# Kernel optimization log

Measured on AMD Instinct MI355X. Metric: run time of the kernel, lower is better.

The kernel has to match this reference:

```python
import jax, jax.numpy as jnp
import numpy as np

P = 8          # patch_size
DIM = 256      # embed dim
HEADS = 8
HEAD_DIM = DIM // HEADS
CH = 3
PATCH_DIM = CH * P * P  # 192
INNER = int(4.0 * DIM)  # 1024
SCALE = HEAD_DIM ** -0.5


def sine_pos_embedding(n, c, dtype=jnp.float32):
    # standard 1D sinusoidal position encoding, shape (n, c)
    pos = jnp.arange(n, dtype=jnp.float32)[:, None]            # (n,1)
    div = jnp.exp(jnp.arange(0, c, 2, dtype=jnp.float32) * (-np.log(10000.0) / c))
    pe = jnp.zeros((n, c), dtype=jnp.float32)
    pe = pe.at[:, 0::2].set(jnp.sin(pos * div))
    pe = pe.at[:, 1::2].set(jnp.cos(pos * div))
    return pe.astype(dtype)


def patchify(x):
    # (B,C,H,W) -> (B, n, p1*p2*C), matching 'b c (h p1) (w p2) -> b (h w) (p1 p2 c)'
    B, C, H, W = x.shape
    hp, wp = H // P, W // P
    x = x.reshape(B, C, hp, P, wp, P)
    x = x.transpose(0, 2, 4, 3, 5, 1)        # (B, hp, wp, p1, p2, C)
    return x.reshape(B, hp * wp, P * P * C)


def unpatchify(x, hp, wp):
    # (B, n, p1*p2*C) -> (B, C, H, W)
    B = x.shape[0]
    x = x.reshape(B, hp, wp, P, P, CH)
    x = x.transpose(0, 5, 1, 3, 2, 4)        # (B, C, hp, p1, wp, p2)
    return x.reshape(B, CH, hp * P, wp * P)


def setup_inputs() -> dict:
    key = jax.random.key(0)
    ks = jax.random.split(key, 16)
    B, H, W = 8, 256, 256
    s = 0.02
    img0 = jax.random.normal(ks[0], (B, CH, H, W), dtype=jnp.float32)
    img1 = jax.random.normal(ks[1], (B, CH, H, W), dtype=jnp.float32)
    mask = jax.random.randint(ks[2], (B, 1, H, W), 0, 2).astype(jnp.float32)
    return {
        "img0": img0,
        "img1": img1,
        "mask": mask,
        "w_patch": jax.random.normal(ks[3], (PATCH_DIM, DIM), jnp.float32) * s,
        "b_patch": jnp.zeros((DIM,), jnp.float32),
        "w_kv": jax.random.normal(ks[4], (DIM, 2 * DIM), jnp.float32) * s,
        "b_kv": jnp.zeros((2 * DIM,), jnp.float32),
        "w_qv": jax.random.normal(ks[5], (DIM, 2 * DIM), jnp.float32) * s,
        "b_qv": jnp.zeros((2 * DIM,), jnp.float32),
        "w_fc1": jax.random.normal(ks[6], (DIM, INNER), jnp.float32) * s,
        "b_fc1": jnp.zeros((INNER,), jnp.float32),
        "w_fc2": jax.random.normal(ks[7], (INNER, PATCH_DIM), jnp.float32) * s,
        "b_fc2": jnp.zeros((PATCH_DIM,), jnp.float32),
    }


def reference(img0, img1, mask, w_patch, b_patch, w_kv, b_kv, w_qv, b_qv,
              w_fc1, b_fc1, w_fc2, b_fc2):
    B, C, H, W = img0.shape
    hp, wp = H // P, W // P
    n = hp * wp

    x0 = patchify(img0) @ w_patch + b_patch   # (B, n, dim)
    x1 = patchify(img1) @ w_patch + b_patch
    pe = sine_pos_embedding(n, DIM)
    x0 = x0 + pe
    x1 = x1 + pe

    # img0 -> k, v
    kv = (x0 @ w_kv + b_kv).reshape(B, n, 2, HEADS, HEAD_DIM)
    kv = kv.transpose(2, 0, 3, 1, 4)          # (2, B, heads, n, hd)
    k, v = kv[0], kv[1]

    # img1 -> q (v1 unused in forward, matching torch code)
    qv = (x1 @ w_qv + b_qv).reshape(B, n, 2, DIM).transpose(2, 0, 1, 3)
    q = qv[0].reshape(B, n, HEADS, HEAD_DIM).transpose(0, 2, 1, 3)  # (B, heads, n, hd)

    dots = jnp.einsum('bhqd,bhkd->bhqk', q, k) * SCALE  # (B, heads, n, n)

    # mask: (B,1,H,W) -> per-patch sum -> binary -> additive bias over key dim
    msum = mask.reshape(B, 1, hp, P, wp, P).sum(axis=(3, 5)).reshape(B, 1, n)
    bias = jnp.where(msum > 0, 0.0, -100.0)[:, :, None, :]  # (B,1,1,n)

    attn = jax.nn.softmax(dots + bias, axis=-1)
    out = jnp.einsum('bhqk,bhkd->bhqd', attn, v)
    out = out.transpose(0, 2, 1, 3).reshape(B, n, DIM)

    # mlp2: Linear -> GELU(exact) -> Linear
    h = jax.nn.gelu(out @ w_fc1 + b_fc1, approximate=False)
    res = h @ w_fc2 + b_fc2                   # (B, n, patch_dim)

    return unpatchify(res, hp, wp)            # (B, C, H, W)
```

## Files before the change

kernel.cpp:

```cpp
#include <hip/hip_runtime.h>
#include <cstdint>
#include <cstddef>

typedef __bf16 bf16_t;
typedef uint32_t u32;
typedef __bf16 bf16x4 __attribute__((ext_vector_type(4)));
typedef __bf16 bf16x8 __attribute__((ext_vector_type(8)));
typedef float f32x4 __attribute__((ext_vector_type(4)));
typedef float f32x16 __attribute__((ext_vector_type(16)));

__device__ __forceinline__ void gload_lds16(const bf16_t* g, bf16_t* l) {
  __builtin_amdgcn_global_load_lds((const __attribute__((address_space(1))) void*)g,
                                   (__attribute__((address_space(3))) void*)l,
                                   16, 0, 0);
}

__device__ __forceinline__ f32x4 mfma16(bf16x8 a, bf16x8 b, f32x4 c) {
  return __builtin_amdgcn_mfma_f32_16x16x32_bf16(a, b, c, 0, 0, 0);
}
__device__ __forceinline__ f32x16 mfma32(bf16x8 a, bf16x8 b, f32x16 c) {
  return __builtin_amdgcn_mfma_f32_32x32x16_bf16(a, b, c, 0, 0, 0);
}

#define LOG2E 1.4426950408889634f

__global__ __launch_bounds__(256)
void prep_all(const float* __restrict__ img0, const float* __restrict__ img1,
              const float* __restrict__ mask,
              const float* __restrict__ wp, const float* __restrict__ wkv,
              const float* __restrict__ wqv, const float* __restrict__ wfc1,
              const float* __restrict__ wfc2,
              bf16_t* __restrict__ xp0, bf16_t* __restrict__ xp1,
              float* __restrict__ pe, float* __restrict__ bias,
              bf16_t* __restrict__ wpT, bf16_t* __restrict__ wkvT,
              bf16_t* __restrict__ wqT, bf16_t* __restrict__ wfc1T,
              bf16_t* __restrict__ wfc2T) {
  __shared__ float tl[64 * 65];
  int bid = blockIdx.x, tid = threadIdx.x;
  if (bid < 1536) {
    int imgsel = bid >= 768;
    int t = (bid - (imgsel ? 768 : 0)) * 256 + tid;
    const float* img = imgsel ? img1 : img0;
    bf16_t* xp = imgsel ? xp1 : xp0;
    int wpp = t & 31, p1 = (t >> 5) & 7, hp = (t >> 8) & 31, rest = t >> 13;
    int b = rest / 3, c = rest - b * 3;
    const float* src = img + (((size_t)(b * 3 + c) * 256 + hp * 8 + p1) * 256 + wpp * 8);
    float4 v0 = *(const float4*)src;
    float4 v1 = *(const float4*)(src + 4);
    int row = b * 1024 + hp * 32 + wpp;
    bf16_t* dst = xp + (size_t)row * 192 + p1 * 24 + c;
    dst[0]  = (bf16_t)v0.x; dst[3]  = (bf16_t)v0.y; dst[6]  = (bf16_t)v0.z; dst[9]  = (bf16_t)v0.w;
    dst[12] = (bf16_t)v1.x; dst[15] = (bf16_t)v1.y; dst[18] = (bf16_t)v1.z; dst[21] = (bf16_t)v1.w;
  } else if (bid < 2560) {
    int t = bid - 1536, c = tid;
    int i2 = c & ~1;
    float div = __expf((float)i2 * (-9.210340371976184f / 256.0f));
    float arg = (float)t * div;
    float sv, cv;
    __sincosf(arg, &sv, &cv);
    pe[t * 256 + c] = (c & 1) ? cv : sv;
  } else if (bid < 2592) {
    int g = (bid - 2560) * 256 + tid;
    int b = g >> 10, t = g & 1023, hp = t >> 5, wpp = t & 31;
    const float* mp = mask + ((size_t)b * 256 + hp * 8) * 256 + wpp * 8;
    float s = 0.f;
    #pragma unroll
    for (int p1 = 0; p1 < 8; p1++) {
      float4 a = *(const float4*)(mp + p1 * 256);
      float4 c = *(const float4*)(mp + p1 * 256 + 4);
      s += a.x + a.y + a.z + a.w + c.x + c.y + c.z + c.w;
    }
    bias[g] = (s > 0.f) ? 0.f : (-100.f * LOG2E);
  } else {
    int i = bid - 2592;
    const float* src; bf16_t* dst; int srcN, dstK, NT;
    if (i >= 172) {
      int j = i - 172;
      bf16_t* p = wfc2T + 192 * 1024 + j * 8192 + tid * 32;
      bf16x8 z;
      #pragma unroll
      for (int e = 0; e < 8; e++) z[e] = (bf16_t)0.0f;
      *(bf16x8*)(p) = z; *(bf16x8*)(p + 8) = z;
      *(bf16x8*)(p + 16) = z; *(bf16x8*)(p + 24) = z;
      return;
    }
    if (i < 12)       { src = wp;   dst = wpT;   srcN = 256;  dstK = 192;  NT = 4; }
    else if (i < 44)  { i -= 12;  src = wkv;  dst = wkvT;  srcN = 512;  dstK = 256;  NT = 8; }
    else if (i < 60)  { i -= 44;  src = wqv;  dst = wqT;   srcN = 512;  dstK = 256;  NT = 4; }
    else if (i < 124) { i -= 60;  src = wfc1; dst = wfc1T; srcN = 1024; dstK = 256;  NT = 16; }
    else              { i -= 124; src = wfc2; dst = wfc2T; srcN = 192;  dstK = 1024; NT = 3; }
    int kt = i / NT, nt = i - kt * NT;
    #pragma unroll
    for (int j = 0; j < 4; j++) {
      int r = (tid >> 4) + 16 * j, c = (tid & 15) * 4;
      float4 v = *(const float4*)(src + (size_t)(kt * 64 + r) * srcN + nt * 64 + c);
      tl[r * 65 + c] = v.x; tl[r * 65 + c + 1] = v.y;
      tl[r * 65 + c + 2] = v.z; tl[r * 65 + c + 3] = v.w;
    }
    __syncthreads();
    #pragma unroll
    for (int j = 0; j < 16; j++) {
      int flat = tid + 256 * j;
      int n_l = flat >> 6, k_l = flat & 63;
      dst[(size_t)(nt * 64 + n_l) * dstK + kt * 64 + k_l] = (bf16_t)tl[k_l * 65 + n_l];
    }
  }
}

template<int EPI, int BN>
__global__ __launch_bounds__(256, 3)
void gemm128d(const bf16_t* __restrict__ A_, const bf16_t* __restrict__ A2,
              const bf16_t* __restrict__ Bt_, const bf16_t* __restrict__ Bt2,
              int M, int N, int K,
              const float* __restrict__ bias_, const float* __restrict__ bias2,
              const float* __restrict__ pe,
              bf16_t* __restrict__ out_b, bf16_t* __restrict__ out_b2,
              bf16_t* __restrict__ out_b3, float* __restrict__ out_f) {
  constexpr int NF = BN / 32;
  __shared__ bf16_t alds[4 * 128 * 8];
  __shared__ bf16_t blds[4 * BN * 8];
  const int tid = threadIdx.x;
  const int lane = tid & 63, wid = tid >> 6;
  const int ln15 = lane & 15, hi = lane >> 4;
  const int brow = blockIdx.x * 128;
  int bcol = blockIdx.y * BN;
  const bf16_t* A = A_;
  const bf16_t* Bt = Bt_;
  const float* bias = bias_;
  bool qpart = false;
  if (EPI == 0 && blockIdx.z) A = A2;
  if (EPI == 5 && blockIdx.y >= 4) {
    qpart = true; A = A2; Bt = Bt2; bias = bias2; bcol -= 512;
  }
  const int wr = wid >> 1, wc = wid & 1;

  f32x4 acc[4][NF];
  #pragma unroll
  for (int m = 0; m < 4; m++)
    #pragma unroll
    for (int n = 0; n < NF; n++) acc[m][n] = (f32x4){0.f, 0.f, 0.f, 0.f};

  for (int k0 = 0; k0 < K; k0 += 32) {
    #pragma unroll
    for (int s = 0; s < 2; s++) {
      int c = tid + s * 256; int kb = c >> 7, row = c & 127;
      gload_lds16(A + (size_t)(brow + row) * K + k0 + kb * 8,
                  &alds[(size_t)(s * 256 + wid * 64) * 8]);
    }
    #pragma unroll
    for (int s = 0; s < BN / 64; s++) {
      int c = tid + s * 256; int kb = c / BN, row = c % BN;
      gload_lds16(Bt + (size_t)(bcol + row) * K + k0 + kb * 8,
                  &blds[(size_t)(s * 256 + wid * 64) * 8]);
    }
    __syncthreads();
    bf16x8 bfr[NF];
    #pragma unroll
    for (int n = 0; n < NF; n++)
      bfr[n] = *(const bf16x8*)&blds[(size_t)(hi * BN + wc * (BN / 2) + n * 16 + ln15) * 8];
    #pragma unroll
    for (int m = 0; m < 4; m++) {
      bf16x8 af = *(const bf16x8*)&alds[(size_t)(hi * 128 + wr * 64 + m * 16 + ln15) * 8];
      #pragma unroll
      for (int n = 0; n < NF; n++)
        acc[m][n] = mfma16(af, bfr[n], acc[m][n]);
    }
    __syncthreads();
  }

  #pragma unroll
  for (int m = 0; m < 4; m++) {
    #pragma unroll
    for (int n = 0; n < NF; n++) {
      #pragma unroll
      for (int r = 0; r < 4; r++) {
        int grow = brow + wr * 64 + m * 16 + hi * 4 + r;
        int gcol = bcol + wc * (BN / 2) + n * 16 + ln15;
        float v = acc[m][n][r];
        if (EPI == 0) {
          v += bias[gcol] + pe[(grow & 1023) * 256 + gcol];
          bf16_t* outx = blockIdx.z ? out_b2 : out_b;
          outx[(size_t)grow * N + gcol] = (bf16_t)v;
        } else if (EPI == 5) {
          v += bias[gcol];
          int b = grow >> 10, t = grow & 1023;
          if (!qpart) {
            if (gcol < 256) {
              int h = gcol >> 5, d = gcol & 31;
              out_b[(((size_t)(b * 8 + h) * 1024 + t) << 5) + d] = (bf16_t)v;
            } else {
              int c2 = gcol - 256; int h = c2 >> 5, d = c2 & 31;
              out_b2[(((size_t)(b * 8 + h) * 32 + d) << 10) + t] = (bf16_t)v;
            }
          } else {
            v *= (0.17677669529663687f * LOG2E);
            int h = gcol >> 5, d = gcol & 31;
            out_b3[(((size_t)(b * 8 + h) * 1024 + t) << 5) + d] = (bf16_t)v;
          }
        } else if (EPI == 3) {
          v += bias[gcol];
          float gg = 0.5f * v * (1.0f + erff(v * 0.7071067811865476f));
          out_b[(size_t)grow * N + gcol] = (bf16_t)gg;
        }
      }
    }
  }
}

template<int BN>
__global__ __launch_bounds__(256)
void gemm_fc2(const bf16_t* __restrict__ A, const bf16_t* __restrict__ Bt,
              int M, int N, int K, const float* __restrict__ bias,
              float* __restrict__ out_f) {
  constexpr int NF = BN / 32;
  __shared__ bf16_t alds[2][8 * 64 * 8];
  __shared__ bf16_t blds[2][8 * BN * 8];
  const int tid = threadIdx.x;
  const int lane = tid & 63, wid = tid >> 6;
  const int ln15 = lane & 15, hi = lane >> 4;
  const int brow = blockIdx.x * 64;
  const int bcol = blockIdx.y * BN;
  const int wr = wid >> 1, wc = wid & 1;

  auto stage = [&](int buf, int k0) {
    #pragma unroll
    for (int s = 0; s < 2; s++) {
      int c = tid + s * 256; int kb = c >> 6, row = c & 63;
      gload_lds16(A + (size_t)(brow + row) * K + k0 + kb * 8,
                  &alds[buf][(size_t)(s * 256 + wid * 64) * 8]);
    }
    #pragma unroll
    for (int s = 0; s < BN / 32; s++) {
      int c = tid + s * 256; int kb = c / BN, row = c & (BN - 1);
      gload_lds16(Bt + (size_t)(bcol + row) * K + k0 + kb * 8,
                  &blds[buf][(size_t)(s * 256 + wid * 64) * 8]);
    }
  };

  f32x4 acc[2][NF];
  #pragma unroll
  for (int m = 0; m < 2; m++)
    #pragma unroll
    for (int n = 0; n < NF; n++) acc[m][n] = (f32x4){0.f, 0.f, 0.f, 0.f};

  stage(0, 0);
  __syncthreads();
  int cur = 0;
  const int NT = K >> 6;
  for (int t = 0; t < NT; t++) {
    if (t + 1 < NT) stage(cur ^ 1, (t + 1) << 6);
    bf16x8 af[2][2], bfr[2][NF];
    #pragma unroll
    for (int kk = 0; kk < 2; kk++) {
      #pragma unroll
      for (int m = 0; m < 2; m++)
        af[kk][m] = *(const bf16x8*)&alds[cur][(size_t)((kk * 4 + hi) * 64 + wr * 32 + m * 16 + ln15) * 8];
      #pragma unroll
      for (int n = 0; n < NF; n++)
        bfr[kk][n] = *(const bf16x8*)&blds[cur][(size_t)((kk * 4 + hi) * BN + wc * (BN / 2) + n * 16 + ln15) * 8];
    }
    #pragma unroll
    for (int kk = 0; kk < 2; kk++)
      #pragma unroll
      for (int m = 0; m < 2; m++)
        #pragma unroll
        for (int n = 0; n < NF; n++)
          acc[m][n] = mfma16(af[kk][m], bfr[kk][n], acc[m][n]);
    __syncthreads();
    cur ^= 1;
  }

  #pragma unroll
  for (int m = 0; m < 2; m++) {
    #pragma unroll
    for (int n = 0; n < NF; n++) {
      #pragma unroll
      for (int r = 0; r < 4; r++) {
        int grow = brow + wr * 32 + m * 16 + hi * 4 + r;
        int gcol = bcol + wc * (BN / 2) + n * 16 + ln15;
        float v = acc[m][n][r] + bias[gcol];
        int b = grow >> 10, t = grow & 1023;
        int hp = t >> 5, wpp = t & 31;
        int p = gcol / 3; int c = gcol - p * 3;
        int p1 = p >> 3, p2 = p & 7;
        out_f[(((size_t)(b * 3 + c) * 256 + hp * 8 + p1) * 256) + wpp * 8 + p2] = v;
      }
    }
  }
}

union PW { u32 w[4]; bf16x8 v; };

__device__ __forceinline__ u32 pkbf(float a, float b) {
  union { bf16_t h[2]; u32 w; } u;
  u.h[0] = (bf16_t)a; u.h[1] = (bf16_t)b;
  return u.w;
}

__device__ __forceinline__ void pl32swap(u32& a, u32& b) {
  asm volatile("v_permlane32_swap_b32 %0, %1" : "+v"(a), "+v"(b));
}

#define SMEM_BYTES 32768

__device__ __forceinline__ void stage_kv(const bf16_t* kbase, const bf16_t* vbase,
                                         int ch, char* smem, int cur,
                                         int tid, int wid) {
  bf16_t* kl = (bf16_t*)(smem + cur * 8192);
  bf16_t* vl = (bf16_t*)(smem + 16384 + cur * 8192);
  #pragma unroll
  for (int s = 0; s < 2; s++) {
    int c = tid + s * 256;
    int row = c >> 2, cs = (c & 3) ^ (row & 3);
    gload_lds16(kbase + (size_t)(ch * 128 + row) * 32 + cs * 8,
                kl + (size_t)(s * 256 + wid * 64) * 8);
  }
  #pragma unroll
  for (int s = 0; s < 2; s++) {
    int c = tid + s * 256;
    int row = c >> 4, cs = (c & 15) ^ (row & 15);
    gload_lds16(vbase + (size_t)row * 1024 + ch * 128 + cs * 8,
                vl + (size_t)(s * 256 + wid * 64) * 8);
  }
}

__global__ __launch_bounds__(256, 4)
void attn_kernel(const bf16_t* __restrict__ q, const bf16_t* __restrict__ k,
                 const bf16_t* __restrict__ vt, const float* __restrict__ bias,
                 bf16_t* __restrict__ out) {
  __shared__ __align__(16) char smem[SMEM_BYTES];

  int tid = threadIdx.x, lane = tid & 63, wid = tid >> 6;
  int l31 = lane & 31, g = lane >> 5;
  int x = blockIdx.x & 7, idx = blockIdx.x >> 3;
  int qt = idx & 31;
  int bh = ((idx >> 5) << 3) | x;
  int b = bh >> 3, h = bh & 7;
  int q0 = qt * 32;
  const bf16_t* qp = q + ((size_t)bh * 1024 + q0 + l31) * 32;
  bf16x8 qf0 = *(const bf16x8*)(qp + g * 8);
  bf16x8 qf1 = *(const bf16x8*)(qp + 16 + g * 8);
  const bf16_t* kbase = k + (size_t)bh * 32768;
  const bf16_t* vbase = vt + (size_t)bh * 32768;
  const float* bb = bias + b * 1024;

  f32x16 acc;
  #pragma unroll
  for (int r = 0; r < 16; r++) acc[r] = 0.f;
  float lsum = 0.f;

  stage_kv(kbase, vbase, 0, smem, 0, tid, wid);
  __syncthreads();

  int cur = 0;
  for (int ch = 0; ch < 8; ch++) {
    if (ch < 7) stage_kv(kbase, vbase, ch + 1, smem, cur ^ 1, tid, wid);
    const bf16_t* kl = (const bf16_t*)(smem + cur * 8192);
    const bf16_t* vl = (const bf16_t*)(smem + 16384 + cur * 8192);
    int base = ch * 128 + wid * 32;
    int row0 = wid * 32 + l31;
    bf16x8 kA = *(const bf16x8*)(kl + (size_t)(row0 * 4 + (g ^ (row0 & 3))) * 8);
    bf16x8 kB = *(const bf16x8*)(kl + (size_t)(row0 * 4 + ((2 + g) ^ (row0 & 3))) * 8);
    bf16x8 vA = *(const bf16x8*)(vl + (size_t)(l31 * 16 + ((wid * 4 + g) ^ (l31 & 15))) * 8);
    bf16x8 vB = *(const bf16x8*)(vl + (size_t)(l31 * 16 + ((wid * 4 + 2 + g) ^ (l31 & 15))) * 8);
    f32x4 c0 = *(const f32x4*)(bb + base + 4 * g);
    f32x4 c1 = *(const f32x4*)(bb + base + 8 + 4 * g);
    f32x4 c2 = *(const f32x4*)(bb + base + 16 + 4 * g);
    f32x4 c3 = *(const f32x4*)(bb + base + 24 + 4 * g);
    f32x16 S;
    S[0] = c0[0]; S[1] = c0[1]; S[2] = c0[2]; S[3] = c0[3];
    S[4] = c1[0]; S[5] = c1[1]; S[6] = c1[2]; S[7] = c1[3];
    S[8] = c2[0]; S[9] = c2[1]; S[10] = c2[2]; S[11] = c2[3];
    S[12] = c3[0]; S[13] = c3[1]; S[14] = c3[2]; S[15] = c3[3];
    S = mfma32(kA, qf0, S);
    S = mfma32(kB, qf1, S);
    float p[16];
    #pragma unroll
    for (int r = 0; r < 16; r++) p[r] = exp2f(S[r]);
    lsum += (((p[0] + p[1]) + (p[2] + p[3])) + ((p[4] + p[5]) + (p[6] + p[7]))) +
            (((p[8] + p[9]) + (p[10] + p[11])) + ((p[12] + p[13]) + (p[14] + p[15])));
    u32 w[8];
    #pragma unroll
    for (int j = 0; j < 8; j++) w[j] = pkbf(p[2 * j], p[2 * j + 1]);
    u32 xa = w[2], ya = w[0]; pl32swap(xa, ya);
    u32 xb = w[3], yb = w[1]; pl32swap(xb, yb);
    u32 xc = w[6], yc = w[4]; pl32swap(xc, yc);
    u32 xd = w[7], yd = w[5]; pl32swap(xd, yd);
    PW A0, A1;
    A0.w[0] = g ? xa : w[0];  A0.w[2] = g ? w[2] : ya;
    A0.w[1] = g ? xb : w[1];  A0.w[3] = g ? w[3] : yb;
    A1.w[0] = g ? xc : w[4];  A1.w[2] = g ? w[6] : yc;
    A1.w[1] = g ? xd : w[5];  A1.w[3] = g ? w[7] : yd;
    acc = mfma32(A0.v, vA, acc);
    acc = mfma32(A1.v, vB, acc);
    __syncthreads();
    cur ^= 1;
  }

  float* OL = (float*)smem;
  float* LS = (float*)(smem + 16896);
  #pragma unroll
  for (int r = 0; r < 16; r++) {
    int row = (r & 3) + 8 * (r >> 2) + 4 * g;
    OL[wid * 1056 + row * 33 + l31] = acc[r];
  }
  lsum += __shfl_xor(lsum, 32);
  LS[wid * 32 + l31] = lsum;
  __syncthreads();

  int qq = tid >> 3, d0 = (tid & 7) * 4;
  float l = LS[qq] + LS[32 + qq] + LS[64 + qq] + LS[96 + qq];
  float o0 = 0.f, o1 = 0.f, o2 = 0.f, o3 = 0.f;
  #pragma unroll
  for (int w2 = 0; w2 < 4; w2++) {
    const float* p = &OL[w2 * 1056 + qq * 33 + d0];
    o0 += p[0]; o1 += p[1]; o2 += p[2]; o3 += p[3];
  }
  float linv = 1.f / l;
  bf16x4 ov;
  ov[0] = (bf16_t)(o0 * linv); ov[1] = (bf16_t)(o1 * linv);
  ov[2] = (bf16_t)(o2 * linv); ov[3] = (bf16_t)(o3 * linv);
  *(bf16x4*)(out + ((size_t)b * 1024 + q0 + qq) * 256 + h * 32 + d0) = ov;
}

extern "C" void kernel_launch(void* const* d_in, const int* in_sizes, int n_in,
                              void* d_out, int out_size, void* d_ws, size_t ws_size,
                              hipStream_t stream) {
  (void)in_sizes; (void)n_in; (void)out_size; (void)ws_size;
  const float* img0    = (const float*)d_in[0];
  const float* img1    = (const float*)d_in[1];
  const float* mask    = (const float*)d_in[2];
  const float* w_patch = (const float*)d_in[3];
  const float* b_patch = (const float*)d_in[4];
  const float* w_kv    = (const float*)d_in[5];
  const float* b_kv    = (const float*)d_in[6];
  const float* w_qv    = (const float*)d_in[7];
  const float* b_qv    = (const float*)d_in[8];
  const float* w_fc1   = (const float*)d_in[9];
  const float* b_fc1   = (const float*)d_in[10];
  const float* w_fc2   = (const float*)d_in[11];
  const float* b_fc2   = (const float*)d_in[12];
  float* out = (float*)d_out;

  char* ws = (char*)d_ws;
  float*  pe    = (float*)(ws + 0);
  float*  bias  = (float*)(ws + 1048576);
  bf16_t* wpT   = (bf16_t*)(ws + 1081344);
  bf16_t* wkvT  = (bf16_t*)(ws + 1179648);
  bf16_t* wqT   = (bf16_t*)(ws + 1441792);
  bf16_t* wfc1T = (bf16_t*)(ws + 1572864);
  bf16_t* wfc2T = (bf16_t*)(ws + 2097152);
  bf16_t* xp0   = (bf16_t*)(ws + 2621440);
  bf16_t* xp1   = (bf16_t*)(ws + 5767168);
  bf16_t* x0    = (bf16_t*)(ws + 8912896);
  bf16_t* x1    = (bf16_t*)(ws + 13107200);
  bf16_t* kbuf  = (bf16_t*)(ws + 17301504);
  bf16_t* vtbuf = (bf16_t*)(ws + 21495808);
  bf16_t* qbuf  = (bf16_t*)(ws + 25690112);
  bf16_t* aout  = (bf16_t*)(ws + 29884416);
  bf16_t* hbuf  = (bf16_t*)(ws + 34078720);

  prep_all<<<2772, 256, 0, stream>>>(img0, img1, mask, w_patch, w_kv, w_qv, w_fc1, w_fc2,
                                     xp0, xp1, pe, bias, wpT, wkvT, wqT, wfc1T, wfc2T);

  gemm128d<0, 64><<<dim3(64, 4, 2), 256, 0, stream>>>(xp0, xp1, wpT, nullptr, 8192, 256, 192,
                                                      b_patch, nullptr, pe, x0, x1, nullptr, nullptr);
  gemm128d<5, 128><<<dim3(64, 6), 256, 0, stream>>>(x0, x1, wkvT, wqT, 8192, 512, 256,
                                                    b_kv, b_qv, nullptr, kbuf, vtbuf, qbuf, nullptr);

  attn_kernel<<<2048, 256, 0, stream>>>(qbuf, kbuf, vtbuf, bias, aout);

  gemm128d<3, 128><<<dim3(64, 8), 256, 0, stream>>>(aout, nullptr, wfc1T, nullptr, 8192, 1024, 256,
                                                    b_fc1, nullptr, nullptr, hbuf, nullptr, nullptr, nullptr);
  gemm_fc2<64><<<dim3(128, 3), 256, 0, stream>>>(hbuf, wfc2T, 8192, 256, 1024, b_fc2, out);
}
```

Baseline: 117.1 us.

## Fold patch embedding into KV/Q projections by precomputing combined weights

Because the patch embedding and the KV/Q projections are both linear, the code now multiplies the weights together in a small prep kernel (W_patch·W_kv and W_patch·W_q). It also precomputes the position-embedding-plus-bias term through the projection, giving per-token bias tables. The separate patch-embed GEMM and its x0/x1 intermediate buffers go away, and the projection GEMM now works directly on patch pixels with K=192. This removes one GEMM launch and its memory traffic. In exchange it adds a small prep GEMM, reads larger bias tables in the epilogue, and rounds the combined weights to bf16, which changes numerics slightly.

```diff
diff --git a/kernel.cpp b/kernel.cpp
--- a/kernel.cpp
+++ b/kernel.cpp
@@ -26,13 +26,13 @@
 
 __global__ __launch_bounds__(256)
 void prep_all(const float* __restrict__ img0, const float* __restrict__ img1,
-              const float* __restrict__ mask,
+              const float* __restrict__ mask, const float* __restrict__ b_patch,
               const float* __restrict__ wp, const float* __restrict__ wkv,
               const float* __restrict__ wqv, const float* __restrict__ wfc1,
               const float* __restrict__ wfc2,
               bf16_t* __restrict__ xp0, bf16_t* __restrict__ xp1,
-              float* __restrict__ pe, float* __restrict__ bias,
-              bf16_t* __restrict__ wpT, bf16_t* __restrict__ wkvT,
+              bf16_t* __restrict__ pe1b, float* __restrict__ bias,
+              bf16_t* __restrict__ wpB, bf16_t* __restrict__ wkvT,
               bf16_t* __restrict__ wqT, bf16_t* __restrict__ wfc1T,
               bf16_t* __restrict__ wfc2T) {
   __shared__ float tl[64 * 65];
@@ -58,7 +58,8 @@
     float arg = (float)t * div;
     float sv, cv;
     __sincosf(arg, &sv, &cv);
-    pe[t * 256 + c] = (c & 1) ? cv : sv;
+    float v = ((c & 1) ? cv : sv) + b_patch[c];
+    pe1b[t * 256 + c] = (bf16_t)v;
   } else if (bid < 2592) {
     int g = (bid - 2560) * 256 + tid;
     int b = g >> 10, t = g & 1023, hp = t >> 5, wpp = t & 31;
@@ -67,8 +68,8 @@
     #pragma unroll
     for (int p1 = 0; p1 < 8; p1++) {
       float4 a = *(const float4*)(mp + p1 * 256);
-      float4 c = *(const float4*)(mp + p1 * 256 + 4);
-      s += a.x + a.y + a.z + a.w + c.x + c.y + c.z + c.w;
+      float4 c2 = *(const float4*)(mp + p1 * 256 + 4);
+      s += a.x + a.y + a.z + a.w + c2.x + c2.y + c2.z + c2.w;
     }
     bias[g] = (s > 0.f) ? 0.f : (-100.f * LOG2E);
   } else {
@@ -84,7 +85,18 @@
       *(bf16x8*)(p + 16) = z; *(bf16x8*)(p + 24) = z;
       return;
     }
-    if (i < 12)       { src = wp;   dst = wpT;   srcN = 256;  dstK = 192;  NT = 4; }
+    if (i < 12) {
+      int base = i * 4096 + tid * 16;
+      const float* s4 = wp + base;
+      bf16_t* d = wpB + base;
+      #pragma unroll
+      for (int j = 0; j < 4; j++) {
+        float4 v = *(const float4*)(s4 + j * 4);
+        d[j * 4 + 0] = (bf16_t)v.x; d[j * 4 + 1] = (bf16_t)v.y;
+        d[j * 4 + 2] = (bf16_t)v.z; d[j * 4 + 3] = (bf16_t)v.w;
+      }
+      return;
+    }
     else if (i < 44)  { i -= 12;  src = wkv;  dst = wkvT;  srcN = 512;  dstK = 256;  NT = 8; }
     else if (i < 60)  { i -= 44;  src = wqv;  dst = wqT;   srcN = 512;  dstK = 256;  NT = 4; }
     else if (i < 124) { i -= 60;  src = wfc1; dst = wfc1T; srcN = 1024; dstK = 256;  NT = 16; }
@@ -103,6 +115,75 @@
       int flat = tid + 256 * j;
       int n_l = flat >> 6, k_l = flat & 63;
       dst[(size_t)(nt * 64 + n_l) * dstK + kt * 64 + k_l] = (bf16_t)tl[k_l * 65 + n_l];
+    }
+  }
+}
+
+__global__ __launch_bounds__(256)
+void prep2(const bf16_t* __restrict__ wkvT, const bf16_t* __restrict__ wqT,
+           const bf16_t* __restrict__ wpB, const bf16_t* __restrict__ pe1b,
+           const float* __restrict__ b_kv, const float* __restrict__ b_qv,
+           bf16_t* __restrict__ wpkvT, bf16_t* __restrict__ wpqT,
+           float* __restrict__ pekv, float* __restrict__ peq) {
+  __shared__ bf16_t alds[4 * 64 * 8];
+  __shared__ bf16_t blds[4 * 64 * 8];
+  const int tid = threadIdx.x;
+  const int lane = tid & 63, wid = tid >> 6;
+  const int ln15 = lane & 15, hi = lane >> 4;
+  const int wr = wid >> 1, wc = wid & 1;
+  const int arow = tid & 63, akb = tid >> 6;
+  const int K = 256;
+
+  int t = blockIdx.x;
+  const bf16_t *A, *B;
+  int bx, by, task;
+  if (t < 24)       { task = 0; bx = t / 3;          by = t - 3 * (t / 3);  A = wkvT; B = wpB; }
+  else if (t < 36)  { task = 1; int i = t - 24;  bx = i / 3; by = i - 3 * (i / 3); A = wqT;  B = wpB; }
+  else if (t < 164) { task = 2; int i = t - 36;  bx = i >> 3; by = i & 7;  A = pe1b; B = wkvT; }
+  else              { task = 3; int i = t - 164; bx = i >> 2; by = i & 3;  A = pe1b; B = wqT; }
+  const int brow = bx * 64, bcol = by * 64;
+
+  f32x4 acc[2][2];
+  #pragma unroll
+  for (int m = 0; m < 2; m++)
+    #pragma unroll
+    for (int n = 0; n < 2; n++) acc[m][n] = (f32x4){0.f, 0.f, 0.f, 0.f};
+
+  for (int k0 = 0; k0 < K; k0 += 32) {
+    gload_lds16(A + (size_t)(brow + arow) * K + k0 + akb * 8,
+                alds + (size_t)(wid * 64) * 8);
+    gload_lds16(B + (size_t)(bcol + arow) * K + k0 + akb * 8,
+                blds + (size_t)(wid * 64) * 8);
+    __syncthreads();
+    bf16x8 af[2], bf[2];
+    #pragma unroll
+    for (int m = 0; m < 2; m++)
+      af[m] = *(const bf16x8*)&alds[(size_t)(hi * 64 + wr * 32 + m * 16 + ln15) * 8];
+    #pragma unroll
+    for (int n = 0; n < 2; n++)
+      bf[n] = *(const bf16x8*)&blds[(size_t)(hi * 64 + wc * 32 + n * 16 + ln15) * 8];
+    #pragma unroll
+    for (int m = 0; m < 2; m++)
+      #pragma unroll
+      for (int n = 0; n < 2; n++)
+        acc[m][n] = mfma16(af[m], bf[n], acc[m][n]);
+    __syncthreads();
+  }
+
+  #pragma unroll
+  for (int m = 0; m < 2; m++) {
+    #pragma unroll
+    for (int n = 0; n < 2; n++) {
+      #pragma unroll
+      for (int r = 0; r < 4; r++) {
+        int grow = brow + wr * 32 + m * 16 + hi * 4 + r;
+        int gcol = bcol + wc * 32 + n * 16 + ln15;
+        float v = acc[m][n][r];
+        if (task == 0)      wpkvT[grow * 192 + gcol] = (bf16_t)v;
+        else if (task == 1) wpqT[grow * 192 + gcol] = (bf16_t)v;
+        else if (task == 2) pekv[grow * 512 + gcol] = v + b_kv[gcol];
+        else                peq[grow * 256 + gcol] = v + b_qv[gcol];
+      }
     }
   }
 }
@@ -113,9 +194,8 @@
               const bf16_t* __restrict__ Bt_, const bf16_t* __restrict__ Bt2,
               int M, int N, int K,
               const float* __restrict__ bias_, const float* __restrict__ bias2,
-              const float* __restrict__ pe,
               bf16_t* __restrict__ out_b, bf16_t* __restrict__ out_b2,
-              bf16_t* __restrict__ out_b3, float* __restrict__ out_f) {
+              bf16_t* __restrict__ out_b3) {
   constexpr int NF = BN / 32;
   __shared__ bf16_t alds[4 * 128 * 8];
   __shared__ bf16_t blds[4 * BN * 8];
@@ -128,8 +208,7 @@
   const bf16_t* Bt = Bt_;
   const float* bias = bias_;
   bool qpart = false;
-  if (EPI == 0 && blockIdx.z) A = A2;
-  if (EPI == 5 && blockIdx.y >= 4) {
+  if (EPI == 7 && blockIdx.y >= 4) {
     qpart = true; A = A2; Bt = Bt2; bias = bias2; bcol -= 512;
   }
   const int wr = wid >> 1, wc = wid & 1;
@@ -177,14 +256,10 @@
         int grow = brow + wr * 64 + m * 16 + hi * 4 + r;
         int gcol = bcol + wc * (BN / 2) + n * 16 + ln15;
         float v = acc[m][n][r];
-        if (EPI == 0) {
-          v += bias[gcol] + pe[(grow & 1023) * 256 + gcol];
-          bf16_t* outx = blockIdx.z ? out_b2 : out_b;
-          outx[(size_t)grow * N + gcol] = (bf16_t)v;
-        } else if (EPI == 5) {
-          v += bias[gcol];
+        if (EPI == 7) {
           int b = grow >> 10, t = grow & 1023;
           if (!qpart) {
+            v += bias[(t << 9) + gcol];
             if (gcol < 256) {
               int h = gcol >> 5, d = gcol & 31;
               out_b[(((size_t)(b * 8 + h) * 1024 + t) << 5) + d] = (bf16_t)v;
@@ -193,7 +268,7 @@
               out_b2[(((size_t)(b * 8 + h) * 32 + d) << 10) + t] = (bf16_t)v;
             }
           } else {
-            v *= (0.17677669529663687f * LOG2E);
+            v = (v + bias[(t << 8) + gcol]) * (0.17677669529663687f * LOG2E);
             int h = gcol >> 5, d = gcol & 31;
             out_b3[(((size_t)(b * 8 + h) * 1024 + t) << 5) + d] = (bf16_t)v;
           }
@@ -443,34 +518,38 @@
   float* out = (float*)d_out;
 
   char* ws = (char*)d_ws;
-  float*  pe    = (float*)(ws + 0);
   float*  bias  = (float*)(ws + 1048576);
-  bf16_t* wpT   = (bf16_t*)(ws + 1081344);
+  bf16_t* wpB   = (bf16_t*)(ws + 1081344);
   bf16_t* wkvT  = (bf16_t*)(ws + 1179648);
   bf16_t* wqT   = (bf16_t*)(ws + 1441792);
   bf16_t* wfc1T = (bf16_t*)(ws + 1572864);
   bf16_t* wfc2T = (bf16_t*)(ws + 2097152);
   bf16_t* xp0   = (bf16_t*)(ws + 2621440);
   bf16_t* xp1   = (bf16_t*)(ws + 5767168);
-  bf16_t* x0    = (bf16_t*)(ws + 8912896);
-  bf16_t* x1    = (bf16_t*)(ws + 13107200);
+  float*  pekv  = (float*)(ws + 8912896);
+  float*  peq   = (float*)(ws + 11010048);
+  bf16_t* pe1b  = (bf16_t*)(ws + 12058624);
+  bf16_t* wpkvT = (bf16_t*)(ws + 12582912);
+  bf16_t* wpqT  = (bf16_t*)(ws + 12779520);
   bf16_t* kbuf  = (bf16_t*)(ws + 17301504);
   bf16_t* vtbuf = (bf16_t*)(ws + 21495808);
   bf16_t* qbuf  = (bf16_t*)(ws + 25690112);
   bf16_t* aout  = (bf16_t*)(ws + 29884416);
   bf16_t* hbuf  = (bf16_t*)(ws + 34078720);
 
-  prep_all<<<2772, 256, 0, stream>>>(img0, img1, mask, w_patch, w_kv, w_qv, w_fc1, w_fc2,
-                                     xp0, xp1, pe, bias, wpT, wkvT, wqT, wfc1T, wfc2T);
-
-  gemm128d<0, 64><<<dim3(64, 4, 2), 256, 0, stream>>>(xp0, xp1, wpT, nullptr, 8192, 256, 192,
-                                                      b_patch, nullptr, pe, x0, x1, nullptr, nullptr);
-  gemm128d<5, 128><<<dim3(64, 6), 256, 0, stream>>>(x0, x1, wkvT, wqT, 8192, 512, 256,
-                                                    b_kv, b_qv, nullptr, kbuf, vtbuf, qbuf, nullptr);
+  prep_all<<<2772, 256, 0, stream>>>(img0, img1, mask, b_patch, w_patch, w_kv, w_qv,
+                                     w_fc1, w_fc2, xp0, xp1, pe1b, bias,
+                                     wpB, wkvT, wqT, wfc1T, wfc2T);
+
+  prep2<<<228, 256, 0, stream>>>(wkvT, wqT, wpB, pe1b, b_kv, b_qv,
+                                 wpkvT, wpqT, pekv, peq);
+
+  gemm128d<7, 128><<<dim3(64, 6), 256, 0, stream>>>(xp0, xp1, wpkvT, wpqT, 8192, 512, 192,
+                                                    pekv, peq, kbuf, vtbuf, qbuf);
 
   attn_kernel<<<2048, 256, 0, stream>>>(qbuf, kbuf, vtbuf, bias, aout);
 
   gemm128d<3, 128><<<dim3(64, 8), 256, 0, stream>>>(aout, nullptr, wfc1T, nullptr, 8192, 1024, 256,
-                                                    b_fc1, nullptr, nullptr, hbuf, nullptr, nullptr, nullptr);
+                                                    b_fc1, nullptr, hbuf, nullptr, nullptr);
   gemm_fc2<64><<<dim3(128, 3), 256, 0, stream>>>(hbuf, wfc2T, 8192, 256, 1024, b_fc2, out);
 }
```

Result: slower. 126.0 us (+7.6%).
